# Kernel optimization log

Hardware: AMD Instinct MI355X
Metric: run time of the kernel (lower is better)

The kernel has to match this reference:

```python
import jax, jax.numpy as jnp
import numpy as np

B_SZ, L, H, P = 8, 8192, 1024, 64  # batch, seq, d_inner, ssm_size
CONJ_SYM = True
DT_MIN, DT_MAX, DT_FLOOR = 1e-3, 1e-1, 1e-4


def setup_inputs() -> dict:
    key = jax.random.key(0)
    ks = jax.random.split(key, 8)
    u = jax.random.normal(ks[0], (B_SZ, L, H), dtype=jnp.float32)
    h_real = jnp.zeros((B_SZ, P), dtype=jnp.float32)
    h_imag = jnp.zeros((B_SZ, P), dtype=jnp.float32)
    # HiPPO-like stable init: Re(Lambda) = -0.5, Im(Lambda) = pi*k
    A_real = -0.5 * jnp.ones((P,), dtype=jnp.float32)
    A_imag = jnp.pi * jnp.arange(P, dtype=jnp.float32)
    local_P = 2 * P if CONJ_SYM else P
    b_scale = np.sqrt(1.0 / local_P).astype(np.float32)
    c_scale = np.sqrt(1.0 / H).astype(np.float32)
    B_real = jax.random.normal(ks[1], (P, H), dtype=jnp.float32) * b_scale
    B_imag = jax.random.normal(ks[2], (P, H), dtype=jnp.float32) * b_scale
    C_real = jax.random.normal(ks[3], (H, P), dtype=jnp.float32) * c_scale
    C_imag = jax.random.normal(ks[4], (H, P), dtype=jnp.float32) * c_scale
    D = jax.random.normal(ks[5], (H,), dtype=jnp.float32)
    # torch init: dt = exp(U(log dt_min, log dt_max)).clamp(dt_floor); inv_dt = dt + log(-expm1(-dt))
    log_dt = jax.random.uniform(ks[6], (P,), dtype=jnp.float32) \
        * (np.log(DT_MAX) - np.log(DT_MIN)) + np.log(DT_MIN)
    dt0 = jnp.clip(jnp.exp(log_dt), DT_FLOOR, None)
    inv_dt = dt0 + jnp.log(-jnp.expm1(-dt0))
    return {"u": u, "h_real": h_real, "h_imag": h_imag,
            "A_real": A_real, "A_imag": A_imag,
            "B_real": B_real, "B_imag": B_imag,
            "C_real": C_real, "C_imag": C_imag,
            "D": D, "inv_dt": inv_dt}


def reference(u, h_real, h_imag, A_real, A_imag, B_real, B_imag,
              C_real, C_imag, D, inv_dt):
    A = A_real + 1j * A_imag            # (P,)
    Bm = B_real + 1j * B_imag           # (P, H)
    Cm = C_real + 1j * C_imag           # (H, P)
    dt = jax.nn.softplus(inv_dt)        # step_rescale = 1.0
    # bilinear discretization
    den = 1.0 - (dt / 2.0) * A
    dA = (1.0 + (dt / 2.0) * A) / den   # (P,)
    dB = (dt / den)[:, None] * Bm       # (P, H)
    # input projection: Bu[b,l,p] = sum_h dB[p,h] * u[b,l,h]
    Bu = jnp.einsum('blh,ph->blp', u, dB)              # complex64 (B, L, P)
    h0 = h_real + 1j * h_imag                          # (B, P)
    Bu = Bu.at[:, 0].add(dA * h0)                      # fold initial state in
    a = jnp.broadcast_to(dA, Bu.shape)
    def combine(e1, e2):
        a1, b1 = e1
        a2, b2 = e2
        return a2 * a1, a2 * b1 + b2
    _, hs = jax.lax.associative_scan(combine, (a, Bu), axis=1)  # (B, L, P)
    yc = jnp.einsum('blp,hp->blh', hs, Cm)
    scale = 2.0 if CONJ_SYM else 1.0
    y = scale * yc.real + D * u
    h_last = hs[:, -1]
    return y, h_last.real, h_last.imag
```

## Files before the change

kernel.cpp:

```cpp
#include <hip/hip_runtime.h>

typedef unsigned short ushort_t;
typedef short s8v __attribute__((ext_vector_type(8)));
typedef unsigned short ushort8 __attribute__((ext_vector_type(8)));
typedef float floatx4 __attribute__((ext_vector_type(4)));

#define MFMA16(a, b, c) __builtin_amdgcn_mfma_f32_16x16x32_bf16((a), (b), (c), 0, 0, 0)

static constexpr int B_SZ = 8;
static constexpr int L = 8192;
static constexpr int H = 1024;
static constexpr int M_TOT = B_SZ * L;
static constexpr int S_CH = 128;
static constexpr int NC = L / S_CH;

__device__ inline ushort_t f2bf(float f) {
    union { float f; unsigned u; } v; v.f = f;
    unsigned r = v.u + 0x7fffu + ((v.u >> 16) & 1u);
    return (ushort_t)(r >> 16);
}

__device__ inline unsigned cvtpk(float lo, float hi) {
    unsigned r;
    asm("v_cvt_pk_bf16_f32 %0, %1, %2" : "=v"(r) : "v"(lo), "v"(hi));
    return r;
}

typedef union { s8v v; unsigned u[4]; } u32x4;

__device__ inline void gload_lds16(const void* g, void* l) {
    __builtin_amdgcn_global_load_lds(
        (const __attribute__((address_space(1))) void*)g,
        (__attribute__((address_space(3))) void*)l, 16, 0, 0);
}

__global__ void params_kernel(const float* __restrict__ A_real,
                              const float* __restrict__ A_imag,
                              const float* __restrict__ inv_dt,
                              float* __restrict__ params,
                              float* __restrict__ dApow) {
    int p = threadIdx.x;
    float x = inv_dt[p];
    float dt = (x > 20.f) ? x : log1pf(expf(x));
    float ar = A_real[p], ai = A_imag[p];
    float dr = 1.f - 0.5f * dt * ar;
    float di = -0.5f * dt * ai;
    float inv = 1.f / fmaf(dr, dr, di * di);
    float nr = 1.f + 0.5f * dt * ar, ni = 0.5f * dt * ai;
    float dAr = (nr * dr + ni * di) * inv;
    float dAi = (ni * dr - nr * di) * inv;
    params[p]       = dAr;
    params[64 + p]  = dAi;
    params[128 + p] = dt * dr * inv;
    params[192 + p] = -dt * di * inv;
    float pr = 1.f, pi = 0.f;
    dApow[2 * p] = 1.f; dApow[2 * p + 1] = 0.f;
    for (int k = 1; k <= S_CH; k++) {
        float npr = pr * dAr - pi * dAi;
        float npi = pr * dAi + pi * dAr;
        pr = npr; pi = npi;
        dApow[k * 128 + 2 * p]     = pr;
        dApow[k * 128 + 2 * p + 1] = pi;
    }
}

__global__ void build_w(const float* __restrict__ Br, const float* __restrict__ Bi,
                        const float* __restrict__ Cr, const float* __restrict__ Ci,
                        const float* __restrict__ params,
                        ushort_t* __restrict__ W1T, ushort_t* __restrict__ CeffT) {
    int t = blockIdx.x * 256 + threadIdx.x;
    if (t < 16384) {
        int ti = t >> 9, g = t & 511;
        int n = g >> 2;
        int qq = (g & 3) ^ ((n >> 1) & 3);
        int kb = ti * 32 + qq * 8;
        int p = n >> 1;
        float sr = params[128 + p], si = params[192 + p];
        ushort8 o;
        #pragma unroll
        for (int e = 0; e < 8; e++) {
            int k = kb + e;
            float br = Br[p * 1024 + k], bi = Bi[p * 1024 + k];
            float v = (n & 1) ? (sr * bi + si * br) : (sr * br - si * bi);
            o[e] = f2bf(v);
        }
        *(ushort8*)&W1T[t * 8] = o;
    } else {
        int t2 = t - 16384;
        int ct_ti = t2 >> 9, g = t2 & 511;
        int ct = ct_ti >> 2, ti = ct_ti & 3;
        int n = g >> 2;
        int h = ct * 128 + n;
        int qq = (g & 3) ^ ((n >> 1) & 3);
        int kb = ti * 32 + qq * 8;
        ushort8 o;
        #pragma unroll
        for (int e = 0; e < 8; e++) {
            int k = kb + e;
            int p = k >> 1;
            float v = (k & 1) ? -2.f * Ci[h * 64 + p] : 2.f * Cr[h * 64 + p];
            o[e] = f2bf(v);
        }
        *(ushort8*)&CeffT[t2 * 8] = o;
    }
}

__global__ __launch_bounds__(256) void gemm1s(const float* __restrict__ u,
                                              const ushort_t* __restrict__ W1T,
                                              const float* __restrict__ params,
                                              const float* __restrict__ dApow,
                                              float* __restrict__ hloc,
                                              float* __restrict__ endbuf) {
    __shared__ ushort_t Blds[32768];
    float* bus = (float*)Blds;
    int tid = threadIdx.x;
    int wave = tid >> 6, lane = tid & 63;
    int q = lane >> 4, mn = lane & 15;
    int swz = q ^ ((mn >> 1) & 3);
    size_t row0 = (size_t)blockIdx.x * 128;

    const float* uA0 = u + (row0 + wave * 32 + mn) * 1024 + q * 8;
    const float* uA1 = uA0 + 16 * 1024;

    floatx4 acc[2][8] = {};

    for (int ph = 0; ph < 4; ph++) {
        if (ph) __syncthreads();
        {
            const ushort_t* gsrc = W1T + (size_t)ph * 32768 + wave * 512 + lane * 8;
            ushort_t* ldst = Blds + wave * 512;
            #pragma unroll
            for (int it = 0; it < 16; it++)
                gload_lds16(gsrc + it * 2048, ldst + it * 2048);
        }
        __syncthreads();
        const float* ua0 = uA0 + ph * 256;
        const float* ua1 = uA1 + ph * 256;
        #pragma unroll
        for (int kt = 0; kt < 8; kt++) {
            float4 f00 = *(const float4*)(ua0 + kt * 32);
            float4 f01 = *(const float4*)(ua0 + kt * 32 + 4);
            float4 f10 = *(const float4*)(ua1 + kt * 32);
            float4 f11 = *(const float4*)(ua1 + kt * 32 + 4);
            u32x4 pa0, pa1;
            pa0.u[0] = cvtpk(f00.x, f00.y); pa0.u[1] = cvtpk(f00.z, f00.w);
            pa0.u[2] = cvtpk(f01.x, f01.y); pa0.u[3] = cvtpk(f01.z, f01.w);
            pa1.u[0] = cvtpk(f10.x, f10.y); pa1.u[1] = cvtpk(f10.z, f10.w);
            pa1.u[2] = cvtpk(f11.x, f11.y); pa1.u[3] = cvtpk(f11.z, f11.w);
            int bofs = kt * 4096 + swz * 8;
            #pragma unroll
            for (int j = 0; j < 8; j++) {
                s8v bf = *(const s8v*)&Blds[bofs + (j * 16 + mn) * 32];
                acc[0][j] = MFMA16(pa0.v, bf, acc[0][j]);
                acc[1][j] = MFMA16(pa1.v, bf, acc[1][j]);
            }
        }
    }
    __syncthreads();
    #pragma unroll
    for (int i = 0; i < 2; i++)
        #pragma unroll
        for (int j = 0; j < 8; j++)
            #pragma unroll
            for (int reg = 0; reg < 4; reg++) {
                int row = wave * 32 + i * 16 + q * 4 + reg;
                bus[row * 128 + j * 16 + mn] = acc[i][j][reg];
            }
    __syncthreads();

    float dAr = params[lane], dAi = params[64 + lane];
    float hr = 0.f, hi = 0.f;
    int base = wave * 32 * 128 + 2 * lane;
    #pragma unroll 8
    for (int t = 0; t < 32; t++) {
        float2 v = *(float2*)&bus[base + t * 128];
        float nhr = fmaf(dAr, hr, fmaf(-dAi, hi, v.x));
        float nhi = fmaf(dAr, hi, fmaf(dAi, hr, v.y));
        hr = nhr; hi = nhi;
        *(float2*)&bus[base + t * 128] = make_float2(hr, hi);
    }
    __syncthreads();

    float a32r = dApow[32 * 128 + 2 * lane], a32i = dApow[32 * 128 + 2 * lane + 1];
    float cr = 0.f, ci = 0.f;
    for (int w2 = 0; w2 < wave; w2++) {
        float2 e = *(float2*)&bus[(w2 * 32 + 31) * 128 + 2 * lane];
        float tr = fmaf(a32r, cr, fmaf(-a32i, ci, e.x));
        float ti = fmaf(a32r, ci, fmaf(a32i, cr, e.y));
        cr = tr; ci = ti;
    }

    float* gbase = hloc + (row0 + wave * 32) * 128 + 2 * lane;
    float lr = 0.f, li = 0.f;
    #pragma unroll 8
    for (int t = 0; t < 32; t++) {
        float2 v = *(float2*)&bus[base + t * 128];
        float pr = dApow[(t + 1) * 128 + 2 * lane];
        float pi = dApow[(t + 1) * 128 + 2 * lane + 1];
        float orr = v.x + pr * cr - pi * ci;
        float oi  = v.y + pr * ci + pi * cr;
        *(float2*)(gbase + (size_t)t * 128) = make_float2(orr, oi);
        lr = orr; li = oi;
    }
    if (wave == 3) {
        float* e = endbuf + (size_t)blockIdx.x * 128 + 2 * lane;
        e[0] = lr; e[1] = li;
    }
}

__global__ void scan_carry(const float* __restrict__ endbuf,
                           const float* __restrict__ dApow,
                           const float* __restrict__ h0r,
                           const float* __restrict__ h0i,
                           float* __restrict__ carry) {
    int t = blockIdx.x * 64 + threadIdx.x;
    int b = t >> 6, p = t & 63;
    float aSr = dApow[S_CH * 128 + 2 * p], aSi = dApow[S_CH * 128 + 2 * p + 1];
    float cr = h0r[b * 64 + p], ci = h0i[b * 64 + p];
    for (int c = 0; c < NC; c++) {
        float* dst = carry + ((size_t)b * NC + c) * 128 + 2 * p;
        dst[0] = cr; dst[1] = ci;
        const float* e = endbuf + ((size_t)b * NC + c) * 128 + 2 * p;
        float er = e[0], ei = e[1];
        float nr = fmaf(aSr, cr, fmaf(-aSi, ci, er));
        float ni = fmaf(aSr, ci, fmaf(aSi, cr, ei));
        cr = nr; ci = ni;
    }
}

__global__ __launch_bounds__(256) void gemm2(const float* __restrict__ hloc,
                                             const ushort_t* __restrict__ CeffT,
                                             const float* __restrict__ u,
                                             const float* __restrict__ D,
                                             const float* __restrict__ dApow,
                                             const float* __restrict__ carry,
                                             float* __restrict__ y,
                                             float* __restrict__ out_hlast) {
    __shared__ ushort_t Blds[32768];
    int tid = threadIdx.x;
    int wave = tid >> 6, lane = tid & 63;
    int q = lane >> 4, mn = lane & 15;
    int swz = q ^ ((mn >> 1) & 3);
    size_t row0 = (size_t)blockIdx.x * 128;
    int b = blockIdx.x >> 6;
    int c = blockIdx.x & 63;

    u32x4 A[2][4];
    #pragma unroll
    for (int i = 0; i < 2; i++) {
        int r_i = wave * 32 + i * 16 + mn;
        int kp = r_i + 1;
        const float* hrow = hloc + (row0 + r_i) * 128;
        const float* prow = dApow + (size_t)kp * 128;
        const float* crow = carry + ((size_t)b * NC + c) * 128;
        bool last = (c == NC - 1) && (r_i == 127);
        #pragma unroll
        for (int kt = 0; kt < 4; kt++) {
            int kb = kt * 32 + q * 8;
            float4 h0 = *(const float4*)(hrow + kb);
            float4 h1 = *(const float4*)(hrow + kb + 4);
            float4 p0 = *(const float4*)(prow + kb);
            float4 p1 = *(const float4*)(prow + kb + 4);
            float4 c0 = *(const float4*)(crow + kb);
            float4 c1 = *(const float4*)(crow + kb + 4);
            float f0 = h0.x + p0.x * c0.x - p0.y * c0.y;
            float f1 = h0.y + p0.x * c0.y + p0.y * c0.x;
            float f2 = h0.z + p0.z * c0.z - p0.w * c0.w;
            float f3 = h0.w + p0.z * c0.w + p0.w * c0.z;
            float f4 = h1.x + p1.x * c1.x - p1.y * c1.y;
            float f5 = h1.y + p1.x * c1.y + p1.y * c1.x;
            float f6 = h1.z + p1.z * c1.z - p1.w * c1.w;
            float f7 = h1.w + p1.z * c1.w + p1.w * c1.z;
            A[i][kt].u[0] = cvtpk(f0, f1); A[i][kt].u[1] = cvtpk(f2, f3);
            A[i][kt].u[2] = cvtpk(f4, f5); A[i][kt].u[3] = cvtpk(f6, f7);
            if (last) {
                int pb = kt * 16 + q * 4;
                out_hlast[b * 64 + pb]           = f0; out_hlast[512 + b * 64 + pb]     = f1;
                out_hlast[b * 64 + pb + 1]       = f2; out_hlast[512 + b * 64 + pb + 1] = f3;
                out_hlast[b * 64 + pb + 2]       = f4; out_hlast[512 + b * 64 + pb + 2] = f5;
                out_hlast[b * 64 + pb + 3]       = f6; out_hlast[512 + b * 64 + pb + 3] = f7;
            }
        }
    }

    for (int ph = 0; ph < 4; ph++) {
        if (ph) __syncthreads();
        {
            const ushort_t* gsrc = CeffT + (size_t)ph * 32768 + wave * 512 + lane * 8;
            ushort_t* ldst = Blds + wave * 512;
            #pragma unroll
            for (int it = 0; it < 16; it++)
                gload_lds16(gsrc + it * 2048, ldst + it * 2048);
        }
        __syncthreads();
        #pragma unroll
        for (int sub = 0; sub < 2; sub++) {
            int ct = ph * 2 + sub;
            floatx4 acc[2][8] = {};
            #pragma unroll
            for (int kt = 0; kt < 4; kt++) {
                int bofs = (sub * 4 + kt) * 4096 + swz * 8;
                #pragma unroll
                for (int j = 0; j < 8; j++) {
                    s8v bf = *(const s8v*)&Blds[bofs + (j * 16 + mn) * 32];
                    acc[0][j] = MFMA16(A[0][kt].v, bf, acc[0][j]);
                    acc[1][j] = MFMA16(A[1][kt].v, bf, acc[1][j]);
                }
            }
            float dv[8];
            #pragma unroll
            for (int j = 0; j < 8; j++) dv[j] = D[ct * 128 + j * 16 + mn];
            #pragma unroll
            for (int i = 0; i < 2; i++)
                #pragma unroll
                for (int j = 0; j < 8; j++) {
                    int col = ct * 128 + j * 16 + mn;
                    #pragma unroll
                    for (int reg = 0; reg < 4; reg++) {
                        size_t row = row0 + wave * 32 + i * 16 + q * 4 + reg;
                        y[row * 1024 + col] = acc[i][j][reg] + dv[j] * u[row * 1024 + col];
                    }
                }
        }
    }
}

extern "C" void kernel_launch(void* const* d_in, const int* in_sizes, int n_in,
                              void* d_out, int out_size, void* d_ws, size_t ws_size,
                              hipStream_t stream) {
    const float* u      = (const float*)d_in[0];
    const float* h_r    = (const float*)d_in[1];
    const float* h_i    = (const float*)d_in[2];
    const float* A_real = (const float*)d_in[3];
    const float* A_imag = (const float*)d_in[4];
    const float* B_real = (const float*)d_in[5];
    const float* B_imag = (const float*)d_in[6];
    const float* C_real = (const float*)d_in[7];
    const float* C_imag = (const float*)d_in[8];
    const float* D      = (const float*)d_in[9];
    const float* inv_dt = (const float*)d_in[10];
    float* out = (float*)d_out;

    float* wsf       = (float*)d_ws;
    float* P_params  = wsf;
    float* P_dApow   = wsf + 1024;
    float* P_carry   = wsf + 1024 + 16640;
    float* P_end     = P_carry + 65536;
    ushort_t* P_W1T  = (ushort_t*)(P_end + 65536);
    ushort_t* P_Ceff = P_W1T + 128 * 1024;
    float* P_Bu      = (float*)(P_Ceff + 1024 * 128);

    params_kernel<<<1, 64, 0, stream>>>(A_real, A_imag, inv_dt, P_params, P_dApow);
    build_w<<<128, 256, 0, stream>>>(B_real, B_imag, C_real, C_imag, P_params, P_W1T, P_Ceff);
    gemm1s<<<M_TOT / 128, 256, 0, stream>>>(u, P_W1T, P_params, P_dApow, P_Bu, P_end);
    scan_carry<<<8, 64, 0, stream>>>(P_end, P_dApow, h_r, h_i, P_carry);
    gemm2<<<M_TOT / 128, 256, 0, stream>>>(P_Bu, P_Ceff, u, D, P_dApow, P_carry,
                                           out, out + (size_t)M_TOT * H);
}
```

Measured before the change: 621.6 us.

## Restage input-projection GEMM through padded LDS tiles and halve gemm2 staging

The first GEMM now stages both the bf16-converted u tile and a row-major W1T slice in padded shared memory every 32 K-elements. Previously it streamed u directly into registers and bulk-loaded swizzled weight phases. build_w is changed to emit the plain row-major weight layout this needs. The carry correction now steps powers of dA by recurrence instead of loading dApow, and gemm2 stages one 128-column C tile at a time so its LDS buffer is halved, which may raise occupancy. In exchange, gemm1s adds a block barrier every 32 K-elements and does software bf16 rounding instead of packed conversion.

```diff
diff --git a/kernel.cpp b/kernel.cpp
--- a/kernel.cpp
+++ b/kernel.cpp
@@ -69,24 +69,15 @@
                         const float* __restrict__ params,
                         ushort_t* __restrict__ W1T, ushort_t* __restrict__ CeffT) {
     int t = blockIdx.x * 256 + threadIdx.x;
-    if (t < 16384) {
-        int ti = t >> 9, g = t & 511;
-        int n = g >> 2;
-        int qq = (g & 3) ^ ((n >> 1) & 3);
-        int kb = ti * 32 + qq * 8;
+    if (t < 128 * 1024) {
+        int n = t >> 10, k = t & 1023;
         int p = n >> 1;
         float sr = params[128 + p], si = params[192 + p];
-        ushort8 o;
-        #pragma unroll
-        for (int e = 0; e < 8; e++) {
-            int k = kb + e;
-            float br = Br[p * 1024 + k], bi = Bi[p * 1024 + k];
-            float v = (n & 1) ? (sr * bi + si * br) : (sr * br - si * bi);
-            o[e] = f2bf(v);
-        }
-        *(ushort8*)&W1T[t * 8] = o;
+        float br = Br[p * 1024 + k], bi = Bi[p * 1024 + k];
+        float v = (n & 1) ? (sr * bi + si * br) : (sr * br - si * bi);
+        W1T[t] = f2bf(v);
     } else {
-        int t2 = t - 16384;
+        int t2 = t - 128 * 1024;
         int ct_ti = t2 >> 9, g = t2 & 511;
         int ct = ct_ti >> 2, ti = ct_ti & 3;
         int n = g >> 2;
@@ -111,49 +102,41 @@
                                               const float* __restrict__ dApow,
                                               float* __restrict__ hloc,
                                               float* __restrict__ endbuf) {
-    __shared__ ushort_t Blds[32768];
-    float* bus = (float*)Blds;
+    __shared__ float bus[128 * 128];
+    ushort_t* As = (ushort_t*)bus;
+    ushort_t* Bs = As + 128 * 40;
     int tid = threadIdx.x;
     int wave = tid >> 6, lane = tid & 63;
     int q = lane >> 4, mn = lane & 15;
-    int swz = q ^ ((mn >> 1) & 3);
     size_t row0 = (size_t)blockIdx.x * 128;
-
-    const float* uA0 = u + (row0 + wave * 32 + mn) * 1024 + q * 8;
-    const float* uA1 = uA0 + 16 * 1024;
+    int r = tid >> 1, half = tid & 1;
 
     floatx4 acc[2][8] = {};
 
-    for (int ph = 0; ph < 4; ph++) {
-        if (ph) __syncthreads();
+    for (int kk = 0; kk < 1024; kk += 32) {
+        __syncthreads();
         {
-            const ushort_t* gsrc = W1T + (size_t)ph * 32768 + wave * 512 + lane * 8;
-            ushort_t* ldst = Blds + wave * 512;
-            #pragma unroll
-            for (int it = 0; it < 16; it++)
-                gload_lds16(gsrc + it * 2048, ldst + it * 2048);
+            const float4* up = (const float4*)(u + (row0 + r) * 1024 + kk + half * 16);
+            float4 f0 = up[0], f1 = up[1], f2 = up[2], f3 = up[3];
+            ushort8 t0, t1;
+            t0[0] = f2bf(f0.x); t0[1] = f2bf(f0.y); t0[2] = f2bf(f0.z); t0[3] = f2bf(f0.w);
+            t0[4] = f2bf(f1.x); t0[5] = f2bf(f1.y); t0[6] = f2bf(f1.z); t0[7] = f2bf(f1.w);
+            t1[0] = f2bf(f2.x); t1[1] = f2bf(f2.y); t1[2] = f2bf(f2.z); t1[3] = f2bf(f2.w);
+            t1[4] = f2bf(f3.x); t1[5] = f2bf(f3.y); t1[6] = f2bf(f3.z); t1[7] = f2bf(f3.w);
+            ushort8* dst = (ushort8*)&As[r * 40 + half * 16];
+            dst[0] = t0; dst[1] = t1;
+            const ushort8* wp = (const ushort8*)(W1T + r * 1024 + kk + half * 16);
+            ushort8* db = (ushort8*)&Bs[r * 40 + half * 16];
+            db[0] = wp[0]; db[1] = wp[1];
         }
         __syncthreads();
-        const float* ua0 = uA0 + ph * 256;
-        const float* ua1 = uA1 + ph * 256;
-        #pragma unroll
-        for (int kt = 0; kt < 8; kt++) {
-            float4 f00 = *(const float4*)(ua0 + kt * 32);
-            float4 f01 = *(const float4*)(ua0 + kt * 32 + 4);
-            float4 f10 = *(const float4*)(ua1 + kt * 32);
-            float4 f11 = *(const float4*)(ua1 + kt * 32 + 4);
-            u32x4 pa0, pa1;
-            pa0.u[0] = cvtpk(f00.x, f00.y); pa0.u[1] = cvtpk(f00.z, f00.w);
-            pa0.u[2] = cvtpk(f01.x, f01.y); pa0.u[3] = cvtpk(f01.z, f01.w);
-            pa1.u[0] = cvtpk(f10.x, f10.y); pa1.u[1] = cvtpk(f10.z, f10.w);
-            pa1.u[2] = cvtpk(f11.x, f11.y); pa1.u[3] = cvtpk(f11.z, f11.w);
-            int bofs = kt * 4096 + swz * 8;
-            #pragma unroll
-            for (int j = 0; j < 8; j++) {
-                s8v bf = *(const s8v*)&Blds[bofs + (j * 16 + mn) * 32];
-                acc[0][j] = MFMA16(pa0.v, bf, acc[0][j]);
-                acc[1][j] = MFMA16(pa1.v, bf, acc[1][j]);
-            }
+        s8v a0 = *(const s8v*)&As[(wave * 32 + mn) * 40 + q * 8];
+        s8v a1 = *(const s8v*)&As[(wave * 32 + 16 + mn) * 40 + q * 8];
+        #pragma unroll
+        for (int j = 0; j < 8; j++) {
+            s8v bf = *(const s8v*)&Bs[(j * 16 + mn) * 40 + q * 8];
+            acc[0][j] = MFMA16(a0, bf, acc[0][j]);
+            acc[1][j] = MFMA16(a1, bf, acc[1][j]);
         }
     }
     __syncthreads();
@@ -192,15 +175,17 @@
 
     float* gbase = hloc + (row0 + wave * 32) * 128 + 2 * lane;
     float lr = 0.f, li = 0.f;
+    float pr = dAr, pi = dAi;
     #pragma unroll 8
     for (int t = 0; t < 32; t++) {
         float2 v = *(float2*)&bus[base + t * 128];
-        float pr = dApow[(t + 1) * 128 + 2 * lane];
-        float pi = dApow[(t + 1) * 128 + 2 * lane + 1];
         float orr = v.x + pr * cr - pi * ci;
         float oi  = v.y + pr * ci + pi * cr;
         *(float2*)(gbase + (size_t)t * 128) = make_float2(orr, oi);
         lr = orr; li = oi;
+        float npr = pr * dAr - pi * dAi;
+        float npi = pr * dAi + pi * dAr;
+        pr = npr; pi = npi;
     }
     if (wave == 3) {
         float* e = endbuf + (size_t)blockIdx.x * 128 + 2 * lane;
@@ -236,7 +221,7 @@
                                              const float* __restrict__ carry,
                                              float* __restrict__ y,
                                              float* __restrict__ out_hlast) {
-    __shared__ ushort_t Blds[32768];
+    __shared__ ushort_t Blds[16384];
     int tid = threadIdx.x;
     int wave = tid >> 6, lane = tid & 63;
     int q = lane >> 4, mn = lane & 15;
@@ -283,45 +268,41 @@
         }
     }
 
-    for (int ph = 0; ph < 4; ph++) {
-        if (ph) __syncthreads();
+    for (int ct = 0; ct < 8; ct++) {
+        if (ct) __syncthreads();
         {
-            const ushort_t* gsrc = CeffT + (size_t)ph * 32768 + wave * 512 + lane * 8;
+            const ushort_t* gsrc = CeffT + (size_t)ct * 16384 + wave * 512 + lane * 8;
             ushort_t* ldst = Blds + wave * 512;
             #pragma unroll
-            for (int it = 0; it < 16; it++)
+            for (int it = 0; it < 8; it++)
                 gload_lds16(gsrc + it * 2048, ldst + it * 2048);
         }
         __syncthreads();
-        #pragma unroll
-        for (int sub = 0; sub < 2; sub++) {
-            int ct = ph * 2 + sub;
-            floatx4 acc[2][8] = {};
+        floatx4 acc[2][8] = {};
+        #pragma unroll
+        for (int kt = 0; kt < 4; kt++) {
+            int bofs = kt * 4096 + swz * 8;
             #pragma unroll
-            for (int kt = 0; kt < 4; kt++) {
-                int bofs = (sub * 4 + kt) * 4096 + swz * 8;
+            for (int j = 0; j < 8; j++) {
+                s8v bf = *(const s8v*)&Blds[bofs + (j * 16 + mn) * 32];
+                acc[0][j] = MFMA16(A[0][kt].v, bf, acc[0][j]);
+                acc[1][j] = MFMA16(A[1][kt].v, bf, acc[1][j]);
+            }
+        }
+        float dv[8];
+        #pragma unroll
+        for (int j = 0; j < 8; j++) dv[j] = D[ct * 128 + j * 16 + mn];
+        #pragma unroll
+        for (int i = 0; i < 2; i++)
+            #pragma unroll
+            for (int j = 0; j < 8; j++) {
+                int col = ct * 128 + j * 16 + mn;
                 #pragma unroll
-                for (int j = 0; j < 8; j++) {
-                    s8v bf = *(const s8v*)&Blds[bofs + (j * 16 + mn) * 32];
-                    acc[0][j] = MFMA16(A[0][kt].v, bf, acc[0][j]);
-                    acc[1][j] = MFMA16(A[1][kt].v, bf, acc[1][j]);
+                for (int reg = 0; reg < 4; reg++) {
+                    size_t row = row0 + wave * 32 + i * 16 + q * 4 + reg;
+                    y[row * 1024 + col] = acc[i][j][reg] + dv[j] * u[row * 1024 + col];
                 }
             }
-            float dv[8];
-            #pragma unroll
-            for (int j = 0; j < 8; j++) dv[j] = D[ct * 128 + j * 16 + mn];
-            #pragma unroll
-            for (int i = 0; i < 2; i++)
-                #pragma unroll
-                for (int j = 0; j < 8; j++) {
-                    int col = ct * 128 + j * 16 + mn;
-                    #pragma unroll
-                    for (int reg = 0; reg < 4; reg++) {
-                        size_t row = row0 + wave * 32 + i * 16 + q * 4 + reg;
-                        y[row * 1024 + col] = acc[i][j][reg] + dv[j] * u[row * 1024 + col];
-                    }
-                }
-        }
     }
 }
 
@@ -351,7 +332,7 @@
     float* P_Bu      = (float*)(P_Ceff + 1024 * 128);
 
     params_kernel<<<1, 64, 0, stream>>>(A_real, A_imag, inv_dt, P_params, P_dApow);
-    build_w<<<128, 256, 0, stream>>>(B_real, B_imag, C_real, C_imag, P_params, P_W1T, P_Ceff);
+    build_w<<<576, 256, 0, stream>>>(B_real, B_imag, C_real, C_imag, P_params, P_W1T, P_Ceff);
     gemm1s<<<M_TOT / 128, 256, 0, stream>>>(u, P_W1T, P_params, P_dApow, P_Bu, P_end);
     scan_carry<<<8, 64, 0, stream>>>(P_end, P_dApow, h_r, h_i, P_carry);
     gemm2<<<M_TOT / 128, 256, 0, stream>>>(P_Bu, P_Ceff, u, D, P_dApow, P_carry,
```

Measured after the change: 752.7 us. 21.1% more time.
